# Optimization experiments

Hardware: AMD Instinct MI355X
Metric: run time of the kernel (lower is better)

## Reference

```python
import jax, jax.numpy as jnp
import numpy as np

N, M, C, F = 100000, 12, 64, 41
SH_DIM = 9  # lmax=2 -> 1+3+5
_INV_SQRT_4PI = 0.28209479177387814  # 1/sqrt(4*pi)


def spherical_harmonics_l2(vec):
    """e3nn real SH, lmax=2, normalize=True, normalization='integral'. vec: [..., 3]."""
    r = jnp.sqrt(jnp.sum(vec * vec, axis=-1, keepdims=True) + 1e-12)
    u = vec / r
    x, y, z = u[..., 0], u[..., 1], u[..., 2]
    s3, s15, s5 = jnp.sqrt(3.0), jnp.sqrt(15.0), jnp.sqrt(5.0)
    sh = jnp.stack([
        jnp.ones_like(x),                              # l=0
        s3 * x, s3 * y, s3 * z,                        # l=1 (e3nn order x,y,z)
        s15 * x * z,                                   # l=2
        s15 * x * y,
        s5 * (y * y - 0.5 * (x * x + z * z)),
        s15 * y * z,
        0.5 * s15 * (z * z - x * x),
    ], axis=-1)
    return sh * _INV_SQRT_4PI  # component -> integral normalization


def setup_inputs() -> dict:
    key = jax.random.key(0)
    ks = jax.random.split(key, 9)
    atom_fea = jax.random.normal(ks[0], (N, C), jnp.float32)
    nbr_fea = jax.random.normal(ks[1], (N, M, F), jnp.float32)
    nbr_idx = jax.random.randint(ks[2], (N, M), 0, N)
    pos = jax.random.normal(ks[3], (N, 3), jnp.float32)
    # radial MLP params (Linear(F,F) -> Softplus -> Linear(F, SH_DIM))
    w1 = jax.random.normal(ks[4], (F, F), jnp.float32) / np.sqrt(F)
    b1 = jnp.zeros((F,), jnp.float32)
    w2 = jax.random.normal(ks[5], (F, SH_DIM), jnp.float32) / np.sqrt(F)
    b2 = jnp.zeros((SH_DIM,), jnp.float32)
    # FullyConnectedTensorProduct weights: single path (0e,0e,0e), uvw -> [C_in, C_out]
    tp_w = jax.random.normal(ks[6], (C, C), jnp.float32)
    return {"atom_fea": atom_fea, "nbr_fea": nbr_fea, "nbr_idx": nbr_idx,
            "pos": pos, "w1": w1, "b1": b1, "w2": w2, "b2": b2, "tp_w": tp_w}


def reference(atom_fea, nbr_fea, nbr_idx, pos, w1, b1, w2, b2, tp_w):
    n, m = nbr_idx.shape
    src = nbr_idx.reshape(-1)                       # [N*M]
    h_j = atom_fea[src]                             # gather: [N*M, C]
    # radial MLP
    R = jax.nn.softplus(nbr_fea.reshape(n * m, -1) @ w1 + b1) @ w2 + b2  # [N*M, 9]
    # spherical harmonics of r_ij (dst is row index i, repeated M times)
    vec = pos[src].reshape(n, m, 3) - pos[:, None, :]
    Y = spherical_harmonics_l2(vec).reshape(n * m, SH_DIM)
    W = R * Y                                       # [N*M, 9]
    # FullyConnectedTensorProduct (Cx0e) x (0e+1o+2e) -> Cx0e: only the
    # scalar (l=0) channel of W couples; path normalization 1/sqrt(fan_in=C).
    msg = (h_j * W[:, :1]) @ (tp_w / np.sqrt(h_j.shape[-1]))  # [N*M, C]
    # scatter-mean with dst = arange(N) repeated M times == mean over M axis
    out = msg.reshape(n, m, -1).mean(axis=1)        # [N, C]
    return out
```

## Files before the change

### kernel.cpp

```cpp
#include <hip/hip_runtime.h>

#define N_ROWS 100000
#define M_NBR  12
#define C_DIM  64
#define F_DIM  41
#define E_TOT  (N_ROWS * M_NBR)

typedef _Float16 half8 __attribute__((ext_vector_type(8)));
typedef float float4v __attribute__((ext_vector_type(4)));

#define WPITCH 72

__global__ __launch_bounds__(256) void edge_mlp_mfma_kernel(
    const float* __restrict__ nbr_fea,
    const float* __restrict__ w1,
    const float* __restrict__ b1,
    const float* __restrict__ w2,
    const float* __restrict__ b2,
    float* __restrict__ s_out)
{
    __shared__ _Float16 Wh[48 * WPITCH];
    __shared__ _Float16 Wl[48 * WPITCH];

    const int tid = threadIdx.x;

    for (int idx = tid; idx < 48 * 64; idx += 256) {
        const int j = idx >> 6, k = idx & 63;
        const float v = (j < F_DIM && k < F_DIM) ? w1[k * F_DIM + j] : 0.0f;
        const _Float16 vh = (_Float16)v;
        Wh[j * WPITCH + k] = vh;
        Wl[j * WPITCH + k] = (_Float16)(v - (float)vh);
    }
    __syncthreads();

    const int lane = tid & 63;
    const int wv   = tid >> 6;
    const int n15  = lane & 15;
    const int g    = lane >> 4;

    half8 Bh[3][2], Bl[3][2];
    #pragma unroll
    for (int nt = 0; nt < 3; ++nt) {
        const int j = nt * 16 + n15;
        #pragma unroll
        for (int ks = 0; ks < 2; ++ks) {
            const int off = j * WPITCH + ks * 32 + g * 8;
            Bh[nt][ks] = *(const half8*)(Wh + off);
            Bl[nt][ks] = *(const half8*)(Wl + off);
        }
    }

    const long e_base = (long)blockIdx.x * 256 + (long)wv * 64;

    float4v acc[4][3];
    #pragma unroll
    for (int mt = 0; mt < 4; ++mt)
        #pragma unroll
        for (int nt = 0; nt < 3; ++nt)
            #pragma unroll
            for (int i = 0; i < 4; ++i) acc[mt][nt][i] = 0.0f;

    #pragma unroll
    for (int ks = 0; ks < 2; ++ks) {
        #pragma unroll
        for (int mt = 0; mt < 4; ++mt) {
            long e = e_base + mt * 16 + n15;
            if (e > (long)E_TOT - 1) e = (long)E_TOT - 1;
            const float* row = nbr_fea + e * F_DIM;
            const int k0 = ks * 32 + g * 8;
            half8 ah, al;
            #pragma unroll
            for (int i = 0; i < 8; ++i) {
                const int k = k0 + i;
                const float v = (k < F_DIM) ? row[k] : 0.0f;
                const _Float16 vh = (_Float16)v;
                ah[i] = vh;
                al[i] = (_Float16)(v - (float)vh);
            }
            #pragma unroll
            for (int nt = 0; nt < 3; ++nt) {
                acc[mt][nt] = __builtin_amdgcn_mfma_f32_16x16x32_f16(ah, Bh[nt][ks], acc[mt][nt], 0, 0, 0);
                acc[mt][nt] = __builtin_amdgcn_mfma_f32_16x16x32_f16(ah, Bl[nt][ks], acc[mt][nt], 0, 0, 0);
                acc[mt][nt] = __builtin_amdgcn_mfma_f32_16x16x32_f16(al, Bh[nt][ks], acc[mt][nt], 0, 0, 0);
                acc[mt][nt] = __builtin_amdgcn_mfma_f32_16x16x32_f16(al, Bl[nt][ks], acc[mt][nt], 0, 0, 0);
            }
        }
    }

    float b1v[3], w2v[3];
    #pragma unroll
    for (int nt = 0; nt < 3; ++nt) {
        const int j = nt * 16 + n15;
        b1v[nt] = (j < F_DIM) ? b1[j] : 0.0f;
        w2v[nt] = (j < F_DIM) ? w2[j * 9] : 0.0f;
    }
    const float b2v   = b2[0];
    const float scale = 0.28209479177387814f / 12.0f;

    #pragma unroll
    for (int mt = 0; mt < 4; ++mt) {
        float p[4];
        #pragma unroll
        for (int r = 0; r < 4; ++r) {
            float sum = 0.0f;
            #pragma unroll
            for (int nt = 0; nt < 3; ++nt) {
                const float v  = acc[mt][nt][r] + b1v[nt];
                const float sp = fmaxf(v, 0.0f) + __logf(1.0f + __expf(-fabsf(v)));
                sum = fmaf(sp, w2v[nt], sum);
            }
            p[r] = sum;
        }
        #pragma unroll
        for (int m = 1; m < 16; m <<= 1) {
            #pragma unroll
            for (int r = 0; r < 4; ++r) p[r] += __shfl_xor(p[r], m, 64);
        }
        if (n15 == 0) {
            #pragma unroll
            for (int r = 0; r < 4; ++r) {
                const long e = e_base + mt * 16 + g * 4 + r;
                if (e < (long)E_TOT) s_out[e] = (p[r] + b2v) * scale;
            }
        }
    }
}

__global__ __launch_bounds__(256) void atom_transform_kernel(
    const float* __restrict__ atom_fea,
    const float* __restrict__ tp_w,
    float* __restrict__ afT)
{
    __shared__ float sA[64 * C_DIM];

    const int tid = threadIdx.x;
    const int c   = tid & 63;
    const int wv  = tid >> 6;

    float Tc[64];
    #pragma unroll
    for (int k = 0; k < 64; ++k) Tc[k] = tp_w[k * 64 + c] * 0.125f;

    const long row0 = (long)blockIdx.x * 64;
    long nrem = (long)N_ROWS - row0;
    const int nrow = nrem < 64 ? (int)nrem : 64;

    {
        const float4* g4 = (const float4*)(atom_fea + row0 * C_DIM);
        float4* l4 = (float4*)sA;
        const int tot4 = nrow * 16;
        for (int i = tid; i < tot4; i += 256) l4[i] = g4[i];
    }
    __syncthreads();

    const int r0 = wv * 16;
    for (int i = 0; i < 16; ++i) {
        int rl = r0 + i;
        if (rl >= nrow) break;
        const float4* ar = (const float4*)(sA + rl * C_DIM);
        float o = 0.0f;
        #pragma unroll
        for (int k4 = 0; k4 < 16; ++k4) {
            float4 a = ar[k4];
            o = fmaf(a.x, Tc[4 * k4 + 0], o);
            o = fmaf(a.y, Tc[4 * k4 + 1], o);
            o = fmaf(a.z, Tc[4 * k4 + 2], o);
            o = fmaf(a.w, Tc[4 * k4 + 3], o);
        }
        afT[(row0 + rl) * C_DIM + c] = o;
    }
}

__global__ __launch_bounds__(256) void gather_kernel(
    const float* __restrict__ afT,
    const int*   __restrict__ nbr_idx,
    const float* __restrict__ s,
    float* __restrict__ out)
{
    const int tid  = threadIdx.x;
    const int lane = tid & 63;
    const int wv   = tid >> 6;
    const int q    = lane >> 4;
    const int c4   = (lane & 15) * 4;

    const int row0 = blockIdx.x * 32 + wv * 8;

    #pragma unroll
    for (int ch = 0; ch < 2; ++ch) {
        int r = row0 + ch * 4 + q;
        const int*   ir = nbr_idx + r * M_NBR;
        const float* sr = s       + r * M_NBR;
        float4 acc = make_float4(0.f, 0.f, 0.f, 0.f);
        #pragma unroll
        for (int j = 0; j < M_NBR; ++j) {
            int   idx = ir[j];
            float sv  = sr[j];
            const float4 a = *(const float4*)(afT + (long)idx * C_DIM + c4);
            acc.x = fmaf(sv, a.x, acc.x);
            acc.y = fmaf(sv, a.y, acc.y);
            acc.z = fmaf(sv, a.z, acc.z);
            acc.w = fmaf(sv, a.w, acc.w);
        }
        *(float4*)(out + (long)r * C_DIM + c4) = acc;
    }
}

__global__ __launch_bounds__(256) void gather_transform_kernel(
    const float* __restrict__ atom_fea,
    const int*   __restrict__ nbr_idx,
    const float* __restrict__ s,
    const float* __restrict__ tp_w,
    float* __restrict__ out)
{
    __shared__ float accL[64 * C_DIM];
    const int tid = threadIdx.x;
    const int c  = tid & 63;
    const int rq = tid >> 6;

    float Tc[64];
    #pragma unroll
    for (int k = 0; k < 64; ++k) Tc[k] = tp_w[k * 64 + c] * 0.125f;

    const int row0 = blockIdx.x * 64;
    for (int i = 0; i < 16; ++i) {
        int r = row0 + rq * 16 + i;
        float a = 0.0f;
        if (r < N_ROWS) {
            const int*   ir = nbr_idx + (long)r * M_NBR;
            const float* sr = s       + (long)r * M_NBR;
            #pragma unroll
            for (int j = 0; j < M_NBR; ++j)
                a = fmaf(sr[j], atom_fea[(long)ir[j] * C_DIM + c], a);
        }
        accL[(rq * 16 + i) * C_DIM + c] = a;
    }
    __syncthreads();
    for (int i = 0; i < 16; ++i) {
        int rl = rq * 16 + i;
        int r  = row0 + rl;
        if (r >= N_ROWS) continue;
        const float* ar = accL + rl * C_DIM;
        float o = 0.0f;
        #pragma unroll
        for (int k = 0; k < 64; ++k) o = fmaf(ar[k], Tc[k], o);
        out[(long)r * C_DIM + c] = o;
    }
}

extern "C" void kernel_launch(void* const* d_in, const int* in_sizes, int n_in,
                              void* d_out, int out_size, void* d_ws, size_t ws_size,
                              hipStream_t stream) {
    const float* atom_fea = (const float*)d_in[0];
    const float* nbr_fea  = (const float*)d_in[1];
    const int*   nbr_idx  = (const int*)  d_in[2];
    const float* w1   = (const float*)d_in[4];
    const float* b1   = (const float*)d_in[5];
    const float* w2   = (const float*)d_in[6];
    const float* b2   = (const float*)d_in[7];
    const float* tp_w = (const float*)d_in[8];

    float* s   = (float*)d_ws;
    float* out = (float*)d_out;

    const int blocksA = (E_TOT + 255) / 256;
    edge_mlp_mfma_kernel<<<blocksA, 256, 0, stream>>>(nbr_fea, w1, b1, w2, b2, s);

    const size_t sBytes   = (size_t)E_TOT * sizeof(float);
    const size_t afTBytes = (size_t)N_ROWS * C_DIM * sizeof(float);

    if (ws_size >= sBytes + afTBytes) {
        float* afT = (float*)((char*)d_ws + sBytes);
        const int blocksT = (N_ROWS + 63) / 64;
        atom_transform_kernel<<<blocksT, 256, 0, stream>>>(atom_fea, tp_w, afT);
        const int blocksG = N_ROWS / 32;
        gather_kernel<<<blocksG, 256, 0, stream>>>(afT, nbr_idx, s, out);
    } else {
        const int blocksB = (N_ROWS + 63) / 64;
        gather_transform_kernel<<<blocksB, 256, 0, stream>>>(atom_fea, nbr_idx, s, tp_w, out);
    }
}
```

Before: 406.2 us.

## Stage edge features through LDS with coalesced loads, drop lo*lo MFMA, MFMA atom transform

The edge MLP kernel now loads each 128-edge tile of nbr_fea with coalesced float4 reads into padded LDS rather than strided per-lane scalar reads from global memory. It also drops the lo*lo correction MFMA from the split-fp16 product. The w1 fragments are built straight from global memory, with no LDS staging. The atom transform is rewritten to use split-fp16 MFMA instead of scalar FMAs. Together these cut uncoalesced global traffic and ALU work, at the cost of slightly lower precision and more LDS per block.

```diff
diff --git a/kernel.cpp b/kernel.cpp
--- a/kernel.cpp
+++ b/kernel.cpp
@@ -9,7 +9,16 @@
 typedef _Float16 half8 __attribute__((ext_vector_type(8)));
 typedef float float4v __attribute__((ext_vector_type(4)));
 
-#define WPITCH 72
+#define EPITCH 68
+
+__device__ __forceinline__ void split8(const float (&v)[8], half8& hi, half8& lo) {
+    #pragma unroll
+    for (int i = 0; i < 8; ++i) {
+        const _Float16 h = (_Float16)v[i];
+        hi[i] = h;
+        lo[i] = (_Float16)(v[i] - (float)h);
+    }
+}
 
 __global__ __launch_bounds__(256) void edge_mlp_mfma_kernel(
     const float* __restrict__ nbr_fea,
@@ -19,24 +28,35 @@
     const float* __restrict__ b2,
     float* __restrict__ s_out)
 {
-    __shared__ _Float16 Wh[48 * WPITCH];
-    __shared__ _Float16 Wl[48 * WPITCH];
-
-    const int tid = threadIdx.x;
-
-    for (int idx = tid; idx < 48 * 64; idx += 256) {
-        const int j = idx >> 6, k = idx & 63;
-        const float v = (j < F_DIM && k < F_DIM) ? w1[k * F_DIM + j] : 0.0f;
-        const _Float16 vh = (_Float16)v;
-        Wh[j * WPITCH + k] = vh;
-        Wl[j * WPITCH + k] = (_Float16)(v - (float)vh);
-    }
-    __syncthreads();
-
+    __shared__ float lx[128 * EPITCH];
+
+    const int tid  = threadIdx.x;
     const int lane = tid & 63;
     const int wv   = tid >> 6;
     const int n15  = lane & 15;
     const int g    = lane >> 4;
+    const long base = (long)blockIdx.x * 128;
+
+    {
+        const float4* g4 = (const float4*)(nbr_fea + base * F_DIM);
+        for (int i = tid; i < 1312; i += 256) {
+            const float4 v = g4[i];
+            const int f = 4 * i;
+            int r = f / F_DIM;
+            int c = f - r * F_DIM;
+            const float vv[4] = {v.x, v.y, v.z, v.w};
+            #pragma unroll
+            for (int t = 0; t < 4; ++t) {
+                lx[r * EPITCH + c] = vv[t];
+                if (++c == F_DIM) { c = 0; ++r; }
+            }
+        }
+        for (int i = tid; i < 128 * 23; i += 256) {
+            const int r = i / 23;
+            const int c = F_DIM + (i - r * 23);
+            lx[r * EPITCH + c] = 0.0f;
+        }
+    }
 
     half8 Bh[3][2], Bl[3][2];
     #pragma unroll
@@ -44,45 +64,42 @@
         const int j = nt * 16 + n15;
         #pragma unroll
         for (int ks = 0; ks < 2; ++ks) {
-            const int off = j * WPITCH + ks * 32 + g * 8;
-            Bh[nt][ks] = *(const half8*)(Wh + off);
-            Bl[nt][ks] = *(const half8*)(Wl + off);
-        }
-    }
-
-    const long e_base = (long)blockIdx.x * 256 + (long)wv * 64;
-
-    float4v acc[4][3];
-    #pragma unroll
-    for (int mt = 0; mt < 4; ++mt)
+            float v[8];
+            #pragma unroll
+            for (int i = 0; i < 8; ++i) {
+                const int k = ks * 32 + g * 8 + i;
+                v[i] = (j < F_DIM && k < F_DIM) ? w1[k * F_DIM + j] : 0.0f;
+            }
+            split8(v, Bh[nt][ks], Bl[nt][ks]);
+        }
+    }
+
+    __syncthreads();
+
+    float4v acc[2][3];
+    #pragma unroll
+    for (int mt = 0; mt < 2; ++mt)
         #pragma unroll
         for (int nt = 0; nt < 3; ++nt)
             #pragma unroll
             for (int i = 0; i < 4; ++i) acc[mt][nt][i] = 0.0f;
 
     #pragma unroll
-    for (int ks = 0; ks < 2; ++ks) {
-        #pragma unroll
-        for (int mt = 0; mt < 4; ++mt) {
-            long e = e_base + mt * 16 + n15;
-            if (e > (long)E_TOT - 1) e = (long)E_TOT - 1;
-            const float* row = nbr_fea + e * F_DIM;
-            const int k0 = ks * 32 + g * 8;
+    for (int mt = 0; mt < 2; ++mt) {
+        const int row = wv * 32 + mt * 16 + n15;
+        #pragma unroll
+        for (int ks = 0; ks < 2; ++ks) {
+            const float* src = lx + row * EPITCH + ks * 32 + g * 8;
+            float av[8];
+            *(float4*)(av)     = *(const float4*)(src);
+            *(float4*)(av + 4) = *(const float4*)(src + 4);
             half8 ah, al;
-            #pragma unroll
-            for (int i = 0; i < 8; ++i) {
-                const int k = k0 + i;
-                const float v = (k < F_DIM) ? row[k] : 0.0f;
-                const _Float16 vh = (_Float16)v;
-                ah[i] = vh;
-                al[i] = (_Float16)(v - (float)vh);
-            }
+            split8(av, ah, al);
             #pragma unroll
             for (int nt = 0; nt < 3; ++nt) {
                 acc[mt][nt] = __builtin_amdgcn_mfma_f32_16x16x32_f16(ah, Bh[nt][ks], acc[mt][nt], 0, 0, 0);
+                acc[mt][nt] = __builtin_amdgcn_mfma_f32_16x16x32_f16(al, Bh[nt][ks], acc[mt][nt], 0, 0, 0);
                 acc[mt][nt] = __builtin_amdgcn_mfma_f32_16x16x32_f16(ah, Bl[nt][ks], acc[mt][nt], 0, 0, 0);
-                acc[mt][nt] = __builtin_amdgcn_mfma_f32_16x16x32_f16(al, Bh[nt][ks], acc[mt][nt], 0, 0, 0);
-                acc[mt][nt] = __builtin_amdgcn_mfma_f32_16x16x32_f16(al, Bl[nt][ks], acc[mt][nt], 0, 0, 0);
             }
         }
     }
@@ -98,7 +115,7 @@
     const float scale = 0.28209479177387814f / 12.0f;
 
     #pragma unroll
-    for (int mt = 0; mt < 4; ++mt) {
+    for (int mt = 0; mt < 2; ++mt) {
         float p[4];
         #pragma unroll
         for (int r = 0; r < 4; ++r) {
@@ -119,55 +136,90 @@
         if (n15 == 0) {
             #pragma unroll
             for (int r = 0; r < 4; ++r) {
-                const long e = e_base + mt * 16 + g * 4 + r;
-                if (e < (long)E_TOT) s_out[e] = (p[r] + b2v) * scale;
-            }
-        }
-    }
-}
-
-__global__ __launch_bounds__(256) void atom_transform_kernel(
+                const long e = base + wv * 32 + mt * 16 + g * 4 + r;
+                s_out[e] = (p[r] + b2v) * scale;
+            }
+        }
+    }
+}
+
+__global__ __launch_bounds__(256) void atom_transform_mfma_kernel(
     const float* __restrict__ atom_fea,
     const float* __restrict__ tp_w,
     float* __restrict__ afT)
 {
-    __shared__ float sA[64 * C_DIM];
-
-    const int tid = threadIdx.x;
-    const int c   = tid & 63;
-    const int wv  = tid >> 6;
-
-    float Tc[64];
-    #pragma unroll
-    for (int k = 0; k < 64; ++k) Tc[k] = tp_w[k * 64 + c] * 0.125f;
-
-    const long row0 = (long)blockIdx.x * 64;
-    long nrem = (long)N_ROWS - row0;
-    const int nrow = nrem < 64 ? (int)nrem : 64;
+    __shared__ float lx[128 * EPITCH];
+
+    const int tid  = threadIdx.x;
+    const int lane = tid & 63;
+    const int wv   = tid >> 6;
+    const int n15  = lane & 15;
+    const int g    = lane >> 4;
+    const long row0 = (long)blockIdx.x * 128;
+    const int nrow = (N_ROWS - row0) < 128 ? (int)(N_ROWS - row0) : 128;
 
     {
         const float4* g4 = (const float4*)(atom_fea + row0 * C_DIM);
-        float4* l4 = (float4*)sA;
-        const int tot4 = nrow * 16;
-        for (int i = tid; i < tot4; i += 256) l4[i] = g4[i];
+        for (int i = tid; i < 128 * 16; i += 256) {
+            const int r  = i >> 4;
+            const int c4 = i & 15;
+            const float4 v = (r < nrow) ? g4[r * 16 + c4] : make_float4(0.f, 0.f, 0.f, 0.f);
+            *(float4*)(lx + r * EPITCH + c4 * 4) = v;
+        }
     }
     __syncthreads();
 
-    const int r0 = wv * 16;
-    for (int i = 0; i < 16; ++i) {
-        int rl = r0 + i;
-        if (rl >= nrow) break;
-        const float4* ar = (const float4*)(sA + rl * C_DIM);
-        float o = 0.0f;
-        #pragma unroll
-        for (int k4 = 0; k4 < 16; ++k4) {
-            float4 a = ar[k4];
-            o = fmaf(a.x, Tc[4 * k4 + 0], o);
-            o = fmaf(a.y, Tc[4 * k4 + 1], o);
-            o = fmaf(a.z, Tc[4 * k4 + 2], o);
-            o = fmaf(a.w, Tc[4 * k4 + 3], o);
-        }
-        afT[(row0 + rl) * C_DIM + c] = o;
+    float4v acc[2][4];
+    #pragma unroll
+    for (int mt = 0; mt < 2; ++mt)
+        #pragma unroll
+        for (int nt = 0; nt < 4; ++nt)
+            #pragma unroll
+            for (int i = 0; i < 4; ++i) acc[mt][nt][i] = 0.0f;
+
+    #pragma unroll
+    for (int ks = 0; ks < 2; ++ks) {
+        half8 Th[4], Tl[4];
+        #pragma unroll
+        for (int nt = 0; nt < 4; ++nt) {
+            const int j = nt * 16 + n15;
+            float v[8];
+            #pragma unroll
+            for (int i = 0; i < 8; ++i) {
+                const int k = ks * 32 + g * 8 + i;
+                v[i] = tp_w[k * C_DIM + j] * 0.125f;
+            }
+            split8(v, Th[nt], Tl[nt]);
+        }
+        #pragma unroll
+        for (int mt = 0; mt < 2; ++mt) {
+            const int row = wv * 32 + mt * 16 + n15;
+            const float* src = lx + row * EPITCH + ks * 32 + g * 8;
+            float av[8];
+            *(float4*)(av)     = *(const float4*)(src);
+            *(float4*)(av + 4) = *(const float4*)(src + 4);
+            half8 ah, al;
+            split8(av, ah, al);
+            #pragma unroll
+            for (int nt = 0; nt < 4; ++nt) {
+                acc[mt][nt] = __builtin_amdgcn_mfma_f32_16x16x32_f16(ah, Th[nt], acc[mt][nt], 0, 0, 0);
+                acc[mt][nt] = __builtin_amdgcn_mfma_f32_16x16x32_f16(al, Th[nt], acc[mt][nt], 0, 0, 0);
+                acc[mt][nt] = __builtin_amdgcn_mfma_f32_16x16x32_f16(ah, Tl[nt], acc[mt][nt], 0, 0, 0);
+            }
+        }
+    }
+
+    #pragma unroll
+    for (int mt = 0; mt < 2; ++mt) {
+        #pragma unroll
+        for (int r = 0; r < 4; ++r) {
+            const long row = row0 + wv * 32 + mt * 16 + g * 4 + r;
+            if (row < N_ROWS) {
+                #pragma unroll
+                for (int nt = 0; nt < 4; ++nt)
+                    afT[row * C_DIM + nt * 16 + n15] = acc[mt][nt][r];
+            }
+        }
     }
 }
 
@@ -262,7 +314,7 @@
     float* s   = (float*)d_ws;
     float* out = (float*)d_out;
 
-    const int blocksA = (E_TOT + 255) / 256;
+    const int blocksA = E_TOT / 128;
     edge_mlp_mfma_kernel<<<blocksA, 256, 0, stream>>>(nbr_fea, w1, b1, w2, b2, s);
 
     const size_t sBytes   = (size_t)E_TOT * sizeof(float);
@@ -270,8 +322,8 @@
 
     if (ws_size >= sBytes + afTBytes) {
         float* afT = (float*)((char*)d_ws + sBytes);
-        const int blocksT = (N_ROWS + 63) / 64;
-        atom_transform_kernel<<<blocksT, 256, 0, stream>>>(atom_fea, tp_w, afT);
+        const int blocksT = (N_ROWS + 127) / 128;
+        atom_transform_mfma_kernel<<<blocksT, 256, 0, stream>>>(atom_fea, tp_w, afT);
         const int blocksG = N_ROWS / 32;
         gather_kernel<<<blocksG, 256, 0, stream>>>(afT, nbr_idx, s, out);
     } else {
```

Measured after the change: 389.3 us. 1.04x faster.
